# Optimization experiments

Hardware: AMD Instinct MI355X
Metric: run time of the kernel (lower is better)

## Reference

```python
import jax, jax.numpy as jnp
import numpy as np
import math

B, S, D, H, R, DFF = 4, 1024, 1024, 16, 64, 4096

def _layernorm(x, g, b, eps=1e-5):
    m = jnp.mean(x, axis=-1, keepdims=True)
    v = jnp.var(x, axis=-1, keepdims=True)
    return (x - m) / jnp.sqrt(v + eps) * g + b

def setup_inputs() -> dict:
    key = jax.random.key(0)
    ks = jax.random.split(key, 12)
    sc = 0.02
    return {
        "src": jax.random.normal(ks[0], (B, S, D), jnp.float32),
        "in_proj_w": jax.random.normal(ks[1], (3 * D, D), jnp.float32) * sc,
        "in_proj_b": jnp.zeros((3 * D,), jnp.float32),
        "out_proj_w": jax.random.normal(ks[2], (D, D), jnp.float32) * sc,
        "out_proj_b": jnp.zeros((D,), jnp.float32),
        "Qp_w": jax.random.normal(ks[3], (R, D), jnp.float32) * sc,
        "Qp_b": jnp.zeros((R,), jnp.float32),
        "Kp_w": jax.random.normal(ks[4], (R, D), jnp.float32) * sc,
        "Kp_b": jnp.zeros((R,), jnp.float32),
        "Vp_w": jax.random.normal(ks[5], (D, D), jnp.float32) * sc,
        "Vp_b": jnp.zeros((D,), jnp.float32),
        "lam": jnp.float32(0.5),
        "ff1_w": jax.random.normal(ks[6], (DFF, D), jnp.float32) * sc,
        "ff1_b": jnp.zeros((DFF,), jnp.float32),
        "ff2_w": jax.random.normal(ks[7], (D, DFF), jnp.float32) * sc,
        "ff2_b": jnp.zeros((D,), jnp.float32),
        "ln1_g": jnp.ones((D,), jnp.float32),
        "ln1_b": jnp.zeros((D,), jnp.float32),
        "ln2_g": jnp.ones((D,), jnp.float32),
        "ln2_b": jnp.zeros((D,), jnp.float32),
    }

def reference(src, in_proj_w, in_proj_b, out_proj_w, out_proj_b,
              Qp_w, Qp_b, Kp_w, Kp_b, Vp_w, Vp_b, lam,
              ff1_w, ff1_b, ff2_w, ff2_b, ln1_g, ln1_b, ln2_g, ln2_b):
    b, s, d = src.shape
    dh = d // H
    # ---- dense multi-head attention (torch nn.MultiheadAttention, eval) ----
    qkv = src @ in_proj_w.T + in_proj_b            # [B,S,3D]
    q, k, v = jnp.split(qkv, 3, axis=-1)
    q = q.reshape(b, s, H, dh).transpose(0, 2, 1, 3)  # [B,H,S,dh]
    k = k.reshape(b, s, H, dh).transpose(0, 2, 1, 3)
    v = v.reshape(b, s, H, dh).transpose(0, 2, 1, 3)
    scores = jnp.einsum('bhqd,bhkd->bhqk', q, k) / math.sqrt(dh)
    attn = jax.nn.softmax(scores, axis=-1)
    ctx = jnp.einsum('bhqk,bhkd->bhqd', attn, v)
    ctx = ctx.transpose(0, 2, 1, 3).reshape(b, s, d)
    dense_output = ctx @ out_proj_w.T + out_proj_b
    # ---- low-rank top-k sparse attention ----
    Q = src @ Qp_w.T + Qp_b                        # [B,S,R]
    K = src @ Kp_w.T + Kp_b
    V = src @ Vp_w.T + Vp_b                        # [B,S,D]
    QK = jnp.einsum('bqr,bkr->bqk', Q, K) / math.sqrt(R)
    aw = jax.nn.softmax(QK, axis=-1)               # [B,S,S]
    kk = max(1, int(s * 0.2))
    topv, topi = jax.lax.top_k(aw, kk)             # [B,S,kk]
    bi = jnp.arange(b)[:, None, None]
    si = jnp.arange(s)[None, :, None]
    sparse_attn = jnp.zeros_like(aw).at[bi, si, topi].set(topv)
    sparse_attn = sparse_attn / (jnp.sum(sparse_attn, axis=-1, keepdims=True) + 1e-9)
    sparse_output = jnp.einsum('bqk,bkd->bqd', sparse_attn, V)
    # ---- fuse, residual, norm, FFN ----
    sig = jax.nn.sigmoid(lam)
    fused = sig * dense_output + (1.0 - sig) * sparse_output
    x = _layernorm(src + fused, ln1_g, ln1_b)
    ff = jax.nn.relu(x @ ff1_w.T + ff1_b) @ ff2_w.T + ff2_b
    return _layernorm(x + ff, ln2_g, ln2_b)
```

## Files before the change

### kernel.cpp

```cpp
#include <hip/hip_runtime.h>
#include <hip/hip_bf16.h>
#include <math.h>
#include <type_traits>

typedef __hip_bfloat16 bf16;
typedef __attribute__((ext_vector_type(8))) short short8;
typedef __attribute__((ext_vector_type(4))) float f32x4;

#define NB 4
#define NS 1024
#define ND 1024
#define NH 16
#define NDH 64
#define NR 64
#define NDFF 4096
#define NM (NB*NS)
#define NTOPK 204

static __device__ __forceinline__ float b2f(bf16 x) { return __bfloat162float(x); }
static __device__ __forceinline__ bf16  f2b(float x) { return __float2bfloat16(x); }
static __device__ __forceinline__ unsigned short bfbits(float x) {
  bf16 h = __float2bfloat16(x);
  return *reinterpret_cast<unsigned short*>(&h);
}

static __device__ __forceinline__ void gload_lds16(const void* g, void* l) {
  __builtin_amdgcn_global_load_lds(
      (const __attribute__((address_space(1))) void*)g,
      (__attribute__((address_space(3))) void*)l, 16, 0, 0);
}

template<int N> static __device__ __forceinline__ void vm_wait() {
  if constexpr (N == 0)       asm volatile("s_waitcnt vmcnt(0)" ::: "memory");
  else if constexpr (N == 2)  asm volatile("s_waitcnt vmcnt(2)" ::: "memory");
  else if constexpr (N == 4)  asm volatile("s_waitcnt vmcnt(4)" ::: "memory");
  else if constexpr (N == 6)  asm volatile("s_waitcnt vmcnt(6)" ::: "memory");
  else if constexpr (N == 8)  asm volatile("s_waitcnt vmcnt(8)" ::: "memory");
  else static_assert(N == 0, "unsupported vmcnt");
}
static __device__ __forceinline__ void bar() {
  asm volatile("s_barrier" ::: "memory");
}

static __device__ __forceinline__ void ld8(const bf16* p, float* d) {
  const uint4 u = *(const uint4*)p;
  d[0] = __uint_as_float((u.x & 0xffffu) << 16);
  d[1] = __uint_as_float(u.x & 0xffff0000u);
  d[2] = __uint_as_float((u.y & 0xffffu) << 16);
  d[3] = __uint_as_float(u.y & 0xffff0000u);
  d[4] = __uint_as_float((u.z & 0xffffu) << 16);
  d[5] = __uint_as_float(u.z & 0xffff0000u);
  d[6] = __uint_as_float((u.w & 0xffffu) << 16);
  d[7] = __uint_as_float(u.w & 0xffff0000u);
}

static __device__ __forceinline__ float block_sum_256(float v, float* rbuf, int tid) {
  rbuf[tid] = v;
  __syncthreads();
  #pragma unroll
  for (int st = 128; st > 0; st >>= 1) {
    if (tid < st) rbuf[tid] += rbuf[tid + st];
    __syncthreads();
  }
  const float r = rbuf[0];
  __syncthreads();
  return r;
}

struct CastArgs {
  const float* in[6];
  bf16* out[6];
  unsigned end[6];
};
__global__ __launch_bounds__(256) void cast6_kernel(CastArgs a) {
  const unsigned b = blockIdx.x;
  int r = 0; unsigned base = 0;
  #pragma unroll
  for (int k = 0; k < 5; ++k)
    if (b >= a.end[k]) { r = k + 1; base = a.end[k]; }
  const float* in = a.in[r];
  bf16* out = a.out[r];
  const unsigned i = ((b - base) * 256 + threadIdx.x) * 4;
  const float4 v = *(const float4*)(in + i);
  uint2 o;
  o.x = (unsigned)bfbits(v.x) | ((unsigned)bfbits(v.y) << 16);
  o.y = (unsigned)bfbits(v.z) | ((unsigned)bfbits(v.w) << 16);
  *(uint2*)(out + i) = o;
}

__global__ __launch_bounds__(256) void pack_qk_kernel(
    const float* __restrict__ Qw, const float* __restrict__ Kw,
    const float* __restrict__ Qb, const float* __restrict__ Kb,
    bf16* __restrict__ w, float* __restrict__ bias) {
  const int r = blockIdx.x;
  const float* srcw = (r < 64) ? (Qw + (size_t)r * ND) : (Kw + (size_t)(r - 64) * ND);
  for (int i = threadIdx.x; i < ND; i += 256) w[(size_t)r * ND + i] = f2b(srcw[i]);
  if (r == 0)
    for (int i = threadIdx.x; i < 128; i += 256)
      bias[i] = (i < 64) ? Qb[i] : Kb[i - 64];
}

template<int BM, int BN, int BK, int BIAS, int RELU, int OUTF32, int OUTT, int VT>
__global__ __launch_bounds__(256) void mfma_gemm(
    const bf16* __restrict__ A, const bf16* __restrict__ W,
    const float* __restrict__ bias, void* __restrict__ C,
    int K, int lda, int ldb, int ldc,
    long long aHi, long long aLo, long long bHi, long long bLo,
    long long cHi, long long cLo, float scale, bf16* __restrict__ C2)
{
  constexpr int WTM = BM / 2;
  constexpr int WTN = BN / 2;
  constexpr int AM = WTM / 16;
  constexpr int AN = WTN / 16;
  constexpr int KK = BK / 32;
  constexpr int SLOTS = BK / 8;
  constexpr int RPC = 512 / BK;
  constexpr int LPW = (BM * BK) / 2048 + (BN * BK) / 2048;
  __shared__ short As[2][BM * BK];
  __shared__ short Bs[2][BN * BK];
  const int tid  = threadIdx.x;
  const int lane = tid & 63;
  const int w    = tid >> 6;
  const int z    = blockIdx.z;
  const long long aOff = (long long)(z >> 4) * aHi + (long long)(z & 15) * aLo;
  const long long bOff = (long long)(z >> 4) * bHi + (long long)(z & 15) * bLo;
  const long long cOff = (long long)(z >> 4) * cHi + (long long)(z & 15) * cLo;

  int bx = blockIdx.x, by = blockIdx.y;
  if ((gridDim.x & 7) == 0) {
    const unsigned lin = blockIdx.y * gridDim.x + blockIdx.x;
    const unsigned Wd = gridDim.x >> 3;
    const unsigned xcd = lin & 7, i = lin >> 3;
    bx = (int)(xcd * Wd + (i % Wd));
    by = (int)(i / Wd);
  }
  const int m0 = by * BM;
  const int n0 = bx * BN;
  const int wr = w >> 1, wc = w & 1;
  const int lm = lane & 15, quad = lane >> 4;

  f32x4 acc[AM][AN];
  #pragma unroll
  for (int i = 0; i < AM; ++i)
    #pragma unroll
    for (int j = 0; j < AN; ++j) acc[i][j] = (f32x4){0.f, 0.f, 0.f, 0.f};

  const int slot = lane & (SLOTS - 1);
  const int sr   = lane / SLOTS;
  const int swz  = (BK == 32) ? ((sr >> 1) & 3) : (sr & 7);
  const int scol = (slot ^ swz) << 3;
  const int xv   = (BK == 32) ? ((lm >> 1) & 3) : (lm & 7);
  const bf16* Ab = A + aOff;
  const bf16* Bb = W + bOff;

  auto stage = [&](int buf, int k0) {
    #pragma unroll
    for (int t = 0; t < (BM * BK) / 2048; ++t) {
      const int row = w * (BM / 4) + t * RPC;
      gload_lds16(Ab + (long long)(m0 + row + sr) * lda + k0 + scol, &As[buf][row * BK]);
    }
    #pragma unroll
    for (int t = 0; t < (BN * BK) / 2048; ++t) {
      const int row = w * (BN / 4) + t * RPC;
      gload_lds16(Bb + (long long)(n0 + row + sr) * ldb + k0 + scol, &Bs[buf][row * BK]);
    }
  };
  auto compute = [&](int buf) {
    #pragma unroll
    for (int kk = 0; kk < KK; ++kk) {
      const int cb = ((kk * 4 + quad) ^ xv) << 3;
      short8 af[AM], bfr[AN];
      #pragma unroll
      for (int i = 0; i < AM; ++i)
        af[i] = *(const short8*)&As[buf][(wr * WTM + i * 16 + lm) * BK + cb];
      #pragma unroll
      for (int j = 0; j < AN; ++j)
        bfr[j] = *(const short8*)&Bs[buf][(wc * WTN + j * 16 + lm) * BK + cb];
      #pragma unroll
      for (int i = 0; i < AM; ++i)
        #pragma unroll
        for (int j = 0; j < AN; ++j)
          acc[i][j] = __builtin_amdgcn_mfma_f32_16x16x32_bf16(af[i], bfr[j], acc[i][j], 0, 0, 0);
    }
  };

  stage(0, 0);
  int cur = 0;
  for (int k0 = BK; k0 < K; k0 += BK) {
    stage(cur ^ 1, k0);
    vm_wait<LPW>();
    bar();
    compute(cur);
    bar();
    cur ^= 1;
  }
  vm_wait<0>();
  bar();
  compute(cur);

  #pragma unroll
  for (int i = 0; i < AM; ++i) {
    #pragma unroll
    for (int j = 0; j < AN; ++j) {
      const int n = n0 + wc * WTN + j * 16 + lm;
      const float bj = BIAS ? bias[n] : 0.f;
      float v0 = acc[i][j][0] * scale + bj;
      float v1 = acc[i][j][1] * scale + bj;
      float v2 = acc[i][j][2] * scale + bj;
      float v3 = acc[i][j][3] * scale + bj;
      if (RELU) {
        v0 = fmaxf(v0, 0.f); v1 = fmaxf(v1, 0.f);
        v2 = fmaxf(v2, 0.f); v3 = fmaxf(v3, 0.f);
      }
      const int mm = m0 + wr * WTM + i * 16 + quad * 4;
      if (VT && n0 >= 2 * ND) {
        const int h = (n - 2 * ND) >> 6, d = (n - 2 * ND) & 63;
        uint2 u;
        u.x = (unsigned)bfbits(v0) | ((unsigned)bfbits(v1) << 16);
        u.y = (unsigned)bfbits(v2) | ((unsigned)bfbits(v3) << 16);
        bf16* dst = C2 + (long long)((mm >> 10) * NH + h) * (NDH * NS)
                       + (long long)d * NS + (mm & 1023);
        *(uint2*)dst = u;
      } else if (OUTT) {
        uint2 u;
        u.x = (unsigned)bfbits(v0) | ((unsigned)bfbits(v1) << 16);
        u.y = (unsigned)bfbits(v2) | ((unsigned)bfbits(v3) << 16);
        bf16* dst = (bf16*)C + cOff + (long long)(mm >> 10) * ((long long)ND * NS)
                       + (long long)n * NS + (mm & 1023);
        *(uint2*)dst = u;
      } else {
        const float vv[4] = {v0, v1, v2, v3};
        #pragma unroll
        for (int rr = 0; rr < 4; ++rr) {
          const long long co = cOff + (long long)(mm + rr) * ldc + n;
          if (OUTF32) ((float*)C)[co] = vv[rr];
          else        ((bf16*)C)[co] = f2b(vv[rr]);
        }
      }
    }
  }
}

template<int BIAS, int RELU, int VT>
__global__ __launch_bounds__(512) void mfma_gemm256(
    const bf16* __restrict__ A, const bf16* __restrict__ W,
    const float* __restrict__ bias, bf16* __restrict__ C,
    int K, int lda, int ldb, int ldc, bf16* __restrict__ C2)
{
  __shared__ short As[2][256 * 64];
  __shared__ short Bs[2][256 * 64];
  const int tid  = threadIdx.x;
  const int lane = tid & 63;
  const int w    = tid >> 6;
  int bx = blockIdx.x, by = blockIdx.y;
  if ((gridDim.x & 7) == 0) {
    const unsigned lin = blockIdx.y * gridDim.x + blockIdx.x;
    const unsigned Wd = gridDim.x >> 3;
    const unsigned xcd = lin & 7, i = lin >> 3;
    bx = (int)(xcd * Wd + (i % Wd));
    by = (int)(i / Wd);
  }
  const int m0 = by * 256;
  const int n0 = bx * 256;
  const int wr = w >> 2, wc = w & 3;
  const int lm = lane & 15, quad = lane >> 4;

  f32x4 acc[8][4];
  #pragma unroll
  for (int i = 0; i < 8; ++i)
    #pragma unroll
    for (int j = 0; j < 4; ++j) acc[i][j] = (f32x4){0.f, 0.f, 0.f, 0.f};

  const int slot = lane & 7, sr = lane >> 3;
  const int scol = (slot ^ sr) << 3;
  const int xv   = lm & 7;

  auto stgA = [&](int buf, int c, int k0) {
    gload_lds16(A + (long long)(m0 + c * 64 + w * 8 + sr) * lda + k0 + scol,
                &As[buf][(c * 64 + w * 8) * 64]);
  };
  auto stgB = [&](int buf, int c, int k0) {
    gload_lds16(W + (long long)(n0 + c * 64 + w * 8 + sr) * ldb + k0 + scol,
                &Bs[buf][(c * 64 + w * 8) * 64]);
  };
  auto dsA = [&](short8* afr, int h, int buf) {
    #pragma unroll
    for (int i = 0; i < 4; ++i)
      #pragma unroll
      for (int kk = 0; kk < 2; ++kk)
        afr[i * 2 + kk] = *(const short8*)
            &As[buf][(wr * 128 + h * 64 + i * 16 + lm) * 64 + (((kk * 4 + quad) ^ xv) << 3)];
  };
  auto dsB = [&](short8* bfr, int jh, int buf) {
    #pragma unroll
    for (int j = 0; j < 2; ++j)
      #pragma unroll
      for (int kk = 0; kk < 2; ++kk)
        bfr[j * 2 + kk] = *(const short8*)
            &Bs[buf][(wc * 64 + jh * 32 + j * 16 + lm) * 64 + (((kk * 4 + quad) ^ xv) << 3)];
  };
  auto mmaq = [&](auto H, auto JH, const short8* afr, const short8* bfr) {
    constexpr int h = decltype(H)::value, jh = decltype(JH)::value;
    __builtin_amdgcn_s_setprio(1);
    #pragma unroll
    for (int i = 0; i < 4; ++i)
      #pragma unroll
      for (int j = 0; j < 2; ++j)
        #pragma unroll
        for (int kk = 0; kk < 2; ++kk)
          acc[h * 4 + i][jh * 2 + j] = __builtin_amdgcn_mfma_f32_16x16x32_bf16(
              afr[i * 2 + kk], bfr[j * 2 + kk], acc[h * 4 + i][jh * 2 + j], 0, 0, 0);
    __builtin_amdgcn_s_setprio(0);
  };
  const std::integral_constant<int, 0> C0{};
  const std::integral_constant<int, 1> C1{};

  stgB(0, 0, 0); stgB(0, 1, 0); stgB(0, 2, 0); stgB(0, 3, 0);
  stgA(0, 0, 0); stgA(0, 2, 0); stgA(0, 1, 0); stgA(0, 3, 0);
  vm_wait<0>();
  bar();

  const int NT = K / 64;
  int p = 0;
  for (int kt = 0; kt < NT; ++kt, p ^= 1) {
    const int k1 = (kt + 1) * 64;
    const bool pre = (kt + 1 < NT);
    short8 afr[8], bfrA[4], bfrB[4];
    dsA(afr, 0, p); dsB(bfrA, 0, p);
    if (pre) { stgB(p ^ 1, 0, k1); stgB(p ^ 1, 1, k1); }
    bar();
    mmaq(C0, C0, afr, bfrA);
    bar();
    dsB(bfrB, 1, p);
    if (pre) { stgB(p ^ 1, 2, k1); stgB(p ^ 1, 3, k1); vm_wait<4>(); }
    else vm_wait<0>();
    bar();
    mmaq(C0, C1, afr, bfrB);
    bar();
    dsA(afr, 1, p);
    if (pre) { stgA(p ^ 1, 0, k1); stgA(p ^ 1, 2, k1); }
    bar();
    mmaq(C1, C0, afr, bfrA);
    bar();
    if (pre) { stgA(p ^ 1, 1, k1); stgA(p ^ 1, 3, k1); vm_wait<2>(); }
    else vm_wait<0>();
    bar();
    mmaq(C1, C1, afr, bfrB);
    bar();
  }

  #pragma unroll
  for (int i = 0; i < 8; ++i) {
    #pragma unroll
    for (int j = 0; j < 4; ++j) {
      const int n = n0 + wc * 64 + j * 16 + lm;
      const float bj = BIAS ? bias[n] : 0.f;
      float v0 = acc[i][j][0] + bj;
      float v1 = acc[i][j][1] + bj;
      float v2 = acc[i][j][2] + bj;
      float v3 = acc[i][j][3] + bj;
      if (RELU) {
        v0 = fmaxf(v0, 0.f); v1 = fmaxf(v1, 0.f);
        v2 = fmaxf(v2, 0.f); v3 = fmaxf(v3, 0.f);
      }
      const int mm = m0 + wr * 128 + i * 16 + quad * 4;
      if (VT && n0 >= 2 * ND) {
        const int h = (n - 2 * ND) >> 6, d = (n - 2 * ND) & 63;
        uint2 u;
        u.x = (unsigned)bfbits(v0) | ((unsigned)bfbits(v1) << 16);
        u.y = (unsigned)bfbits(v2) | ((unsigned)bfbits(v3) << 16);
        bf16* dst = C2 + (long long)((mm >> 10) * NH + h) * (NDH * NS)
                       + (long long)d * NS + (mm & 1023);
        *(uint2*)dst = u;
      } else {
        C[(long long)(mm + 0) * ldc + n] = f2b(v0);
        C[(long long)(mm + 1) * ldc + n] = f2b(v1);
        C[(long long)(mm + 2) * ldc + n] = f2b(v2);
        C[(long long)(mm + 3) * ldc + n] = f2b(v3);
      }
    }
  }
}

__global__ __launch_bounds__(256) void attn_kernel(
    const bf16* __restrict__ qkv,
    const bf16* __restrict__ Vt,
    bf16* __restrict__ ctx)
{
  __shared__ short smem[2][2][64 * 64];
  const int tid = threadIdx.x, lane = tid & 63, w = tid >> 6;
  const int lm = lane & 15, quad = lane >> 4;
  const int z = blockIdx.y, b = z >> 4, h = z & 15;
  const int q0 = blockIdx.x * 128;
  const bf16* Qb = qkv + (long long)b * NS * 3072 + h * 64;
  const bf16* Kb = Qb + ND;
  const bf16* Vb = Vt + (long long)z * (NDH * NS);

  short8 qf[2][2];
  #pragma unroll
  for (int j = 0; j < 2; ++j)
    #pragma unroll
    for (int kk = 0; kk < 2; ++kk)
      qf[j][kk] = *(const short8*)(Qb + (long long)(q0 + w * 32 + j * 16 + lm) * 3072
                                      + kk * 32 + quad * 8);

  const int slot = lane & 7, sr = lane >> 3;
  const int scol = (slot ^ sr) << 3;

  auto stage = [&](int buf, int t) {
    #pragma unroll
    for (int u = 0; u < 2; ++u) {
      const int row = w * 16 + u * 8;
      gload_lds16(Kb + (long long)(t * 64 + row + sr) * 3072 + scol,
                  &smem[buf][0][row * 64]);
    }
    #pragma unroll
    for (int u = 0; u < 2; ++u) {
      const int row = w * 16 + u * 8;
      gload_lds16(Vb + (long long)(row + sr) * NS + t * 64 + scol,
                  &smem[buf][1][row * 64]);
    }
  };

  f32x4 o[4][2];
  #pragma unroll
  for (int i = 0; i < 4; ++i)
    #pragma unroll
    for (int j = 0; j < 2; ++j) o[i][j] = (f32x4){0.f, 0.f, 0.f, 0.f};
  float m[2] = {-1e30f, -1e30f}, l[2] = {0.f, 0.f};

  stage(0, 0);
  for (int t = 0; t < 16; ++t) {
    const int buf = t & 1;
    if (t < 15) { stage(buf ^ 1, t + 1); vm_wait<4>(); }
    else        { vm_wait<0>(); }
    bar();

    f32x4 st[4][2];
    #pragma unroll
    for (int i = 0; i < 4; ++i)
      #pragma unroll
      for (int j = 0; j < 2; ++j) st[i][j] = (f32x4){0.f, 0.f, 0.f, 0.f};
    #pragma unroll
    for (int kk = 0; kk < 2; ++kk) {
      const int cb = ((kk * 4 + quad) ^ (lm & 7)) << 3;
      short8 ka[4];
      #pragma unroll
      for (int i = 0; i < 4; ++i)
        ka[i] = *(const short8*)&smem[buf][0][(i * 16 + lm) * 64 + cb];
      #pragma unroll
      for (int i = 0; i < 4; ++i)
        #pragma unroll
        for (int j = 0; j < 2; ++j)
          st[i][j] = __builtin_amdgcn_mfma_f32_16x16x32_bf16(ka[i], qf[j][kk], st[i][j], 0, 0, 0);
    }

    #pragma unroll
    for (int j = 0; j < 2; ++j) {
      float pm = -1e30f;
      #pragma unroll
      for (int i = 0; i < 4; ++i)
        #pragma unroll
        for (int r = 0; r < 4; ++r) {
          st[i][j][r] *= 0.125f;
          pm = fmaxf(pm, st[i][j][r]);
        }
      pm = fmaxf(pm, __shfl_xor(pm, 16, 64));
      pm = fmaxf(pm, __shfl_xor(pm, 32, 64));
      const float mn = fmaxf(m[j], pm);
      const float sc = __expf(m[j] - mn);
      float ps = 0.f;
      #pragma unroll
      for (int i = 0; i < 4; ++i)
        #pragma unroll
        for (int r = 0; r < 4; ++r) {
          const float e = __expf(st[i][j][r] - mn);
          st[i][j][r] = e;
          ps += e;
        }
      ps += __shfl_xor(ps, 16, 64);
      ps += __shfl_xor(ps, 32, 64);
      l[j] = l[j] * sc + ps;
      m[j] = mn;
      #pragma unroll
      for (int i = 0; i < 4; ++i)
        #pragma unroll
        for (int r = 0; r < 4; ++r) o[i][j][r] *= sc;
    }

    unsigned u0[4][2], u1[4][2];
    #pragma unroll
    for (int i = 0; i < 4; ++i)
      #pragma unroll
      for (int j = 0; j < 2; ++j) {
        u0[i][j] = (unsigned)bfbits(st[i][j][0]) | ((unsigned)bfbits(st[i][j][1]) << 16);
        u1[i][j] = (unsigned)bfbits(st[i][j][2]) | ((unsigned)bfbits(st[i][j][3]) << 16);
      }
    const int s0l = ((quad & 1) * 2) * 16 + lm;
    const int s1l = s0l + 16;
    const bool hi = (quad >> 1) != 0;

    #pragma unroll
    for (int kk = 0; kk < 2; ++kk) {
      short8 pf[2];
      #pragma unroll
      for (int j = 0; j < 2; ++j) {
        const unsigned a0 = __shfl(u0[kk * 2][j],     s0l, 64);
        const unsigned a1 = __shfl(u1[kk * 2][j],     s0l, 64);
        const unsigned b0 = __shfl(u0[kk * 2 + 1][j], s0l, 64);
        const unsigned b1 = __shfl(u1[kk * 2 + 1][j], s0l, 64);
        const unsigned c0 = __shfl(u0[kk * 2][j],     s1l, 64);
        const unsigned c1 = __shfl(u1[kk * 2][j],     s1l, 64);
        const unsigned d0 = __shfl(u0[kk * 2 + 1][j], s1l, 64);
        const unsigned d1 = __shfl(u1[kk * 2 + 1][j], s1l, 64);
        union { uint4 u; short8 s; } cv;
        cv.u.x = hi ? b0 : a0; cv.u.y = hi ? b1 : a1;
        cv.u.z = hi ? d0 : c0; cv.u.w = hi ? d1 : c1;
        pf[j] = cv.s;
      }
      const int cb = ((kk * 4 + quad) ^ (lm & 7)) << 3;
      short8 va[4];
      #pragma unroll
      for (int i = 0; i < 4; ++i)
        va[i] = *(const short8*)&smem[buf][1][(i * 16 + lm) * 64 + cb];
      #pragma unroll
      for (int i = 0; i < 4; ++i)
        #pragma unroll
        for (int j = 0; j < 2; ++j)
          o[i][j] = __builtin_amdgcn_mfma_f32_16x16x32_bf16(va[i], pf[j], o[i][j], 0, 0, 0);
    }
    bar();
  }

  short (*OL)[72] = (short(*)[72])&smem[0][0][0];
  #pragma unroll
  for (int j = 0; j < 2; ++j) {
    const float inv = 1.f / l[j];
    #pragma unroll
    for (int i = 0; i < 4; ++i) {
      uint2 u;
      u.x = (unsigned)bfbits(o[i][j][0] * inv) | ((unsigned)bfbits(o[i][j][1] * inv) << 16);
      u.y = (unsigned)bfbits(o[i][j][2] * inv) | ((unsigned)bfbits(o[i][j][3] * inv) << 16);
      *(uint2*)&OL[w * 32 + j * 16 + lm][i * 16 + quad * 4] = u;
    }
  }
  __syncthreads();
  {
    const int q = tid >> 1, c = (tid & 1) * 32;
    const uint4 r0 = *(const uint4*)&OL[q][c];
    const uint4 r1 = *(const uint4*)&OL[q][c + 8];
    const uint4 r2 = *(const uint4*)&OL[q][c + 16];
    const uint4 r3 = *(const uint4*)&OL[q][c + 24];
    bf16* dst = ctx + ((long long)(b * NS + q0 + q)) * 1024 + h * 64 + c;
    ((uint4*)dst)[0] = r0; ((uint4*)dst)[1] = r1;
    ((uint4*)dst)[2] = r2; ((uint4*)dst)[3] = r3;
  }
}

__global__ __launch_bounds__(256) void sparse_select_kernel(
    const float* __restrict__ S, bf16* __restrict__ aw)
{
  __shared__ unsigned hist[4][256];
  const int tid = threadIdx.x;
  const int lane = tid & 63;
  const int wv = tid >> 6;
  const long long row = (long long)blockIdx.x * 4 + wv;

  float sv[16];
  const float* sp = S + row * 1024 + lane * 16;
  #pragma unroll
  for (int c = 0; c < 4; ++c) {
    const float4 v = ((const float4*)sp)[c];
    sv[4*c] = v.x; sv[4*c+1] = v.y; sv[4*c+2] = v.z; sv[4*c+3] = v.w;
  }
  unsigned key[16];
  #pragma unroll
  for (int j = 0; j < 16; ++j) {
    const unsigned u = __float_as_uint(sv[j]);
    key[j] = (u & 0x80000000u) ? ~u : (u | 0x80000000u);
  }

  unsigned pref = 0u;
  int need = NTOPK;
  #pragma unroll
  for (int p = 3; p >= 0; --p) {
    *(uint4*)&hist[wv][lane * 4] = (uint4){0u, 0u, 0u, 0u};
    __syncthreads();
    const int sh = (p + 1) * 8;
    #pragma unroll
    for (int j = 0; j < 16; ++j) {
      const bool part = (p == 3) || ((key[j] >> sh) == pref);
      if (part) atomicAdd(&hist[wv][(key[j] >> (p * 8)) & 255u], 1u);
    }
    __syncthreads();
    const unsigned h0 = hist[wv][4*lane],     h1 = hist[wv][4*lane + 1];
    const unsigned h2 = hist[wv][4*lane + 2], h3 = hist[wv][4*lane + 3];
    const unsigned s3 = h3, s2 = h2 + s3, s1 = h1 + s2, s0 = h0 + s1;
    unsigned sum = s0;
    #pragma unroll
    for (int d2 = 1; d2 < 64; d2 <<= 1) {
      const unsigned t = __shfl_down(sum, d2, 64);
      if (lane < 64 - d2) sum += t;
    }
    const unsigned above = sum - s0;
    const unsigned cum[4]  = {above + s0, above + s1, above + s2, above + s3};
    const unsigned next[4] = {above + s1, above + s2, above + s3, above};
    unsigned candPref = 0u; int candNeed = 0; bool has = false;
    #pragma unroll
    for (int i = 0; i < 4; ++i) {
      if ((int)cum[i] >= need && (int)next[i] < need) {
        has = true;
        candPref = (pref << 8) | (unsigned)(4 * lane + i);
        candNeed = need - (int)next[i];
      }
    }
    const unsigned long long m = __ballot(has);
    const int srcLane = (int)(__ffsll((long long)m) - 1);
    pref = (unsigned)__shfl((int)candPref, srcLane, 64);
    need = __shfl(candNeed, srcLane, 64);
  }

  const unsigned T = pref;
  const unsigned tb = (T & 0x80000000u) ? (T ^ 0x80000000u) : ~T;
  const float thr = __uint_as_float(tb);

  float wvv[16];
  float psTop = 0.f, psAll = 0.f;
  #pragma unroll
  for (int j = 0; j < 16; ++j) {
    const float e = __expf(sv[j] - thr);
    psAll += e;
    const float wt = (key[j] >= T) ? e : 0.f;
    psTop += wt;
    wvv[j] = wt;
  }
  #pragma unroll
  for (int s = 1; s < 64; s <<= 1) {
    psTop += __shfl_xor(psTop, s, 64);
    psAll += __shfl_xor(psAll, s, 64);
  }
  const float inv = 1.f / (psTop + 1e-9f * psAll);

  uint4 o0, o1;
  o0.x = (unsigned)bfbits(wvv[0]*inv)  | ((unsigned)bfbits(wvv[1]*inv)  << 16);
  o0.y = (unsigned)bfbits(wvv[2]*inv)  | ((unsigned)bfbits(wvv[3]*inv)  << 16);
  o0.z = (unsigned)bfbits(wvv[4]*inv)  | ((unsigned)bfbits(wvv[5]*inv)  << 16);
  o0.w = (unsigned)bfbits(wvv[6]*inv)  | ((unsigned)bfbits(wvv[7]*inv)  << 16);
  o1.x = (unsigned)bfbits(wvv[8]*inv)  | ((unsigned)bfbits(wvv[9]*inv)  << 16);
  o1.y = (unsigned)bfbits(wvv[10]*inv) | ((unsigned)bfbits(wvv[11]*inv) << 16);
  o1.z = (unsigned)bfbits(wvv[12]*inv) | ((unsigned)bfbits(wvv[13]*inv) << 16);
  o1.w = (unsigned)bfbits(wvv[14]*inv) | ((unsigned)bfbits(wvv[15]*inv) << 16);
  bf16* op = aw + row * 1024 + lane * 16;
  ((uint4*)op)[0] = o0; ((uint4*)op)[1] = o1;
}

__global__ __launch_bounds__(256) void fuse_ln1_kernel(
    const float* __restrict__ src, const bf16* __restrict__ dense,
    const bf16* __restrict__ sparse, const float* __restrict__ lam,
    const float* __restrict__ g, const float* __restrict__ beta,
    bf16* __restrict__ x1)
{
  __shared__ float y[ND];
  __shared__ float rbuf[256];
  const int tid = threadIdx.x;
  const size_t base = (size_t)blockIdx.x * ND;
  const float sig = 1.f / (1.f + __expf(-lam[0]));
  const float c1 = 1.f - sig;
  float s1 = 0.f, s2 = 0.f;
  #pragma unroll
  for (int j = 0; j < 4; ++j) {
    const int i = tid + (j << 8);
    const float v = src[base + i] + sig * b2f(dense[base + i]) + c1 * b2f(sparse[base + i]);
    y[i] = v; s1 += v; s2 += v * v;
  }
  const float sum1 = block_sum_256(s1, rbuf, tid);
  const float sum2 = block_sum_256(s2, rbuf, tid);
  const float mean = sum1 * (1.f / ND);
  const float var  = sum2 * (1.f / ND) - mean * mean;
  const float rstd = rsqrtf(var + 1e-5f);
  #pragma unroll
  for (int j = 0; j < 4; ++j) {
    const int i = tid + (j << 8);
    x1[base + i] = f2b((y[i] - mean) * rstd * g[i] + beta[i]);
  }
}

__global__ __launch_bounds__(256) void ln2_kernel(
    const bf16* __restrict__ x1, const bf16* __restrict__ ff,
    const float* __restrict__ g, const float* __restrict__ beta,
    float* __restrict__ outp)
{
  __shared__ float y[ND];
  __shared__ float rbuf[256];
  const int tid = threadIdx.x;
  const size_t base = (size_t)blockIdx.x * ND;
  float s1 = 0.f, s2 = 0.f;
  #pragma unroll
  for (int j = 0; j < 4; ++j) {
    const int i = tid + (j << 8);
    const float v = b2f(x1[base + i]) + b2f(ff[base + i]);
    y[i] = v; s1 += v; s2 += v * v;
  }
  const float sum1 = block_sum_256(s1, rbuf, tid);
  const float sum2 = block_sum_256(s2, rbuf, tid);
  const float mean = sum1 * (1.f / ND);
  const float var  = sum2 * (1.f / ND) - mean * mean;
  const float rstd = rsqrtf(var + 1e-5f);
  #pragma unroll
  for (int j = 0; j < 4; ++j) {
    const int i = tid + (j << 8);
    outp[base + i] = (y[i] - mean) * rstd * g[i] + beta[i];
  }
}

extern "C" void kernel_launch(void* const* d_in, const int* in_sizes, int n_in,
                              void* d_out, int out_size, void* d_ws, size_t ws_size,
                              hipStream_t stream)
{
  const float* src        = (const float*)d_in[0];
  const float* in_proj_w  = (const float*)d_in[1];
  const float* in_proj_b  = (const float*)d_in[2];
  const float* out_proj_w = (const float*)d_in[3];
  const float* out_proj_b = (const float*)d_in[4];
  const float* Qp_w  = (const float*)d_in[5];
  const float* Qp_b  = (const float*)d_in[6];
  const float* Kp_w  = (const float*)d_in[7];
  const float* Kp_b  = (const float*)d_in[8];
  const float* Vp_w  = (const float*)d_in[9];
  const float* Vp_b  = (const float*)d_in[10];
  const float* lam   = (const float*)d_in[11];
  const float* ff1_w = (const float*)d_in[12];
  const float* ff1_b = (const float*)d_in[13];
  const float* ff2_w = (const float*)d_in[14];
  const float* ff2_b = (const float*)d_in[15];
  const float* ln1_g = (const float*)d_in[16];
  const float* ln1_b = (const float*)d_in[17];
  const float* ln2_g = (const float*)d_in[18];
  const float* ln2_b = (const float*)d_in[19];
  (void)in_sizes; (void)n_in; (void)out_size; (void)ws_size;

  char* ws = (char*)d_ws;
  size_t off = 0;
  auto take = [&](size_t bytes) -> void* {
    void* p = ws + off; off += (bytes + 255) & ~(size_t)255; return p;
  };
  bf16*  src_bf  = (bf16*) take((size_t)NM * ND * 2);
  bf16*  w_qkv   = (bf16*) take((size_t)3 * ND * ND * 2);
  bf16*  w_out   = (bf16*) take((size_t)ND * ND * 2);
  bf16*  w_vp    = (bf16*) take((size_t)ND * ND * 2);
  bf16*  w_ff1   = (bf16*) take((size_t)NDFF * ND * 2);
  bf16*  w_ff2   = (bf16*) take((size_t)ND * NDFF * 2);
  bf16*  w_qk    = (bf16*) take((size_t)128 * ND * 2);
  float* bias_qk = (float*)take(128 * 4);
  const size_t mark = off;
  bf16*  qkv     = (bf16*) take((size_t)NM * 3 * ND * 2);
  bf16*  Vt_all  = (bf16*) take((size_t)NH * NS * NS * 2);
  bf16*  Vt_old  = (bf16*) take((size_t)NH * NDH * NS * 2);
  bf16*  ctx     = (bf16*) take((size_t)NM * ND * 2);
  bf16*  dense   = (bf16*) take((size_t)NM * ND * 2);
  bf16*  QKs_bf  = (bf16*) take((size_t)NM * 128 * 2);
  bf16*  Vsp     = (bf16*) take((size_t)NM * ND * 2);
  bf16*  sparse  = (bf16*) take((size_t)NM * ND * 2);
  (void)Vt_old; (void)Vsp;
  bf16*  x1    = (bf16*)(ws + mark);
  bf16*  h1    = (bf16*)(ws + mark + (size_t)NM * ND * 2);
  bf16*  ffout = (bf16*)(ws + mark + (size_t)NM * ND * 2 + (size_t)NM * NDFF * 2);
  bf16*  aw    = (bf16*)(ws + mark + 2 * (size_t)NM * ND * 2 + (size_t)NM * NDFF * 2);
  float* S_sp  = (float*)(ws + mark + (size_t)NM * ND * 2);
  bf16*  Vsp_t = (bf16*)ctx;

  const dim3 blk(256);
  bf16* const NOC2 = nullptr;
  {
    CastArgs a;
    a.in[0] = src;        a.out[0] = src_bf;
    a.in[1] = in_proj_w;  a.out[1] = w_qkv;
    a.in[2] = out_proj_w; a.out[2] = w_out;
    a.in[3] = Vp_w;       a.out[3] = w_vp;
    a.in[4] = ff1_w;      a.out[4] = w_ff1;
    a.in[5] = ff2_w;      a.out[5] = w_ff2;
    a.end[0] = 4096; a.end[1] = 7168; a.end[2] = 8192;
    a.end[3] = 9216; a.end[4] = 13312; a.end[5] = 17408;
    cast6_kernel<<<dim3(17408), blk, 0, stream>>>(a);
  }
  pack_qk_kernel<<<dim3(128), blk, 0, stream>>>(Qp_w, Kp_w, Qp_b, Kp_b, w_qk, bias_qk);

  mfma_gemm256<1,0,1><<<dim3(3*ND/256, NM/256), dim3(512), 0, stream>>>(
      src_bf, w_qkv, in_proj_b, qkv, ND, ND, ND, 3*ND, Vt_all);

  attn_kernel<<<dim3(NS/128, NB*NH), blk, 0, stream>>>(qkv, Vt_all, ctx);

  mfma_gemm<128,64,64,1,0,0,0,0><<<dim3(ND/64, NM/128, 1), blk, 0, stream>>>(
      ctx, w_out, out_proj_b, dense, ND, ND, ND, ND, 0,0, 0,0, 0,0, 1.f, NOC2);
  mfma_gemm<128,64,64,1,0,0,0,0><<<dim3(2, NM/128, 1), blk, 0, stream>>>(
      src_bf, w_qk, bias_qk, QKs_bf, ND, ND, ND, 128, 0,0, 0,0, 0,0, 1.f, NOC2);
  mfma_gemm<128,64,64,0,0,1,0,0><<<dim3(NS/64, NS/128, NB), blk, 0, stream>>>(
      QKs_bf, QKs_bf + 64, nullptr, S_sp, 64, 128, 128, NS,
      0, (long long)NS*128, 0, (long long)NS*128, 0, (long long)NS*NS, 0.125f, NOC2);
  mfma_gemm<128,64,64,1,0,0,1,0><<<dim3(ND/64, NM/128, 1), blk, 0, stream>>>(
      src_bf, w_vp, Vp_b, Vsp_t, ND, ND, ND, NS, 0,0, 0,0, 0,0, 1.f, NOC2);
  sparse_select_kernel<<<dim3(NM/4), blk, 0, stream>>>(S_sp, aw);
  mfma_gemm<128,64,64,0,0,0,0,0><<<dim3(ND/64, NS/128, NB), blk, 0, stream>>>(
      aw, Vsp_t, nullptr, sparse, NS, NS, NS, ND,
      0, (long long)NS*ND, 0, (long long)ND*NS, 0, (long long)NS*ND, 1.f, NOC2);
  fuse_ln1_kernel<<<dim3(NM), blk, 0, stream>>>(src, dense, sparse, lam, ln1_g, ln1_b, x1);
  mfma_gemm256<1,1,0><<<dim3(NDFF/256, NM/256), dim3(512), 0, stream>>>(
      x1, w_ff1, ff1_b, h1, ND, ND, ND, NDFF, NOC2);
  mfma_gemm<128,64,64,1,0,0,0,0><<<dim3(ND/64, NM/128, 1), blk, 0, stream>>>(
      h1, w_ff2, ff2_b, ffout, NDFF, NDFF, NDFF, ND, 0,0, 0,0, 0,0, 1.f, NOC2);
  ln2_kernel<<<dim3(NM), blk, 0, stream>>>(x1, ffout, ln2_g, ln2_b, (float*)d_out);
}
```

Measured before the change: 424.3 us.

## Pre-pack B operands into MFMA fragment layout and load them directly to registers

Adds a pack kernel that casts the out_proj, Vp and ff2 weights into a layout that matches 16x32 MFMA fragments. A new GEMM variant reads these packed B tiles straight from global memory into registers with one 16-byte load per lane, and stages only A through LDS. The Vp projection now writes its output in the same packed layout, so the sparse-attention GEMM can use the same path. This removes LDS staging and bank traffic for B and shrinks the general cast kernel, at the cost of extra pack launches and B loads that are less coalesced.

```diff
diff --git a/kernel.cpp b/kernel.cpp
--- a/kernel.cpp
+++ b/kernel.cpp
@@ -88,6 +88,23 @@
   *(uint2*)(out + i) = o;
 }
 
+__global__ __launch_bounds__(256) void pack_w_kernel(
+    const float* __restrict__ W, bf16* __restrict__ out, int K) {
+  const int lane = threadIdx.x & 63, sub = threadIdx.x >> 6;
+  const int kt2 = blockIdx.x * 4 + sub;
+  const int nt  = blockIdx.y;
+  const int lm = lane & 15, quad = lane >> 4;
+  const float* p = W + (size_t)(nt * 16 + lm) * K + kt2 * 32 + quad * 8;
+  const float4 a = *(const float4*)p;
+  const float4 b = *(const float4*)(p + 4);
+  uint4 o;
+  o.x = (unsigned)bfbits(a.x) | ((unsigned)bfbits(a.y) << 16);
+  o.y = (unsigned)bfbits(a.z) | ((unsigned)bfbits(a.w) << 16);
+  o.z = (unsigned)bfbits(b.x) | ((unsigned)bfbits(b.y) << 16);
+  o.w = (unsigned)bfbits(b.z) | ((unsigned)bfbits(b.w) << 16);
+  *(uint4*)(out + (((size_t)(nt * (K >> 5) + kt2)) << 9) + lane * 8) = o;
+}
+
 __global__ __launch_bounds__(256) void pack_qk_kernel(
     const float* __restrict__ Qw, const float* __restrict__ Kw,
     const float* __restrict__ Qb, const float* __restrict__ Kb,
@@ -100,13 +117,13 @@
       bias[i] = (i < 64) ? Qb[i] : Kb[i - 64];
 }
 
-template<int BM, int BN, int BK, int BIAS, int RELU, int OUTF32, int OUTT, int VT>
+template<int BM, int BN, int BK, int BIAS, int RELU, int OUTF32>
 __global__ __launch_bounds__(256) void mfma_gemm(
     const bf16* __restrict__ A, const bf16* __restrict__ W,
     const float* __restrict__ bias, void* __restrict__ C,
     int K, int lda, int ldb, int ldc,
     long long aHi, long long aLo, long long bHi, long long bLo,
-    long long cHi, long long cLo, float scale, bf16* __restrict__ C2)
+    long long cHi, long long cLo, float scale)
 {
   constexpr int WTM = BM / 2;
   constexpr int WTN = BN / 2;
@@ -204,38 +221,136 @@
     for (int j = 0; j < AN; ++j) {
       const int n = n0 + wc * WTN + j * 16 + lm;
       const float bj = BIAS ? bias[n] : 0.f;
-      float v0 = acc[i][j][0] * scale + bj;
-      float v1 = acc[i][j][1] * scale + bj;
-      float v2 = acc[i][j][2] * scale + bj;
-      float v3 = acc[i][j][3] * scale + bj;
+      #pragma unroll
+      for (int rr = 0; rr < 4; ++rr) {
+        const int m = m0 + wr * WTM + i * 16 + quad * 4 + rr;
+        float v = acc[i][j][rr] * scale + bj;
+        if (RELU) v = fmaxf(v, 0.f);
+        const long long co = cOff + (long long)m * ldc + n;
+        if (OUTF32) ((float*)C)[co] = v;
+        else        ((bf16*)C)[co] = f2b(v);
+      }
+    }
+  }
+}
+
+template<int BIAS, int RELU, int PACKOUT>
+__global__ __launch_bounds__(256) void mfma_gemm_pb(
+    const bf16* __restrict__ A, const bf16* __restrict__ Bp,
+    const float* __restrict__ bias, bf16* __restrict__ C,
+    int K, int lda, int ldc,
+    long long aLo, long long bLo, long long cLo)
+{
+  __shared__ short As[2][128 * 64];
+  const int tid = threadIdx.x, lane = tid & 63, w = tid >> 6;
+  const int z = blockIdx.z;
+  const long long aOff = (long long)z * aLo;
+  const long long cOff = (long long)z * cLo;
+  int bx = blockIdx.x, by = blockIdx.y;
+  if ((gridDim.x & 7) == 0) {
+    const unsigned lin = blockIdx.y * gridDim.x + blockIdx.x;
+    const unsigned Wd = gridDim.x >> 3;
+    const unsigned xcd = lin & 7, i = lin >> 3;
+    bx = (int)(xcd * Wd + (i % Wd));
+    by = (int)(i / Wd);
+  }
+  const int m0 = by * 128, n0 = bx * 64;
+  const int wr = w >> 1, wc = w & 1;
+  const int lm = lane & 15, quad = lane >> 4;
+  const int KT2 = K >> 5;
+
+  f32x4 acc[4][2];
+  #pragma unroll
+  for (int i = 0; i < 4; ++i)
+    #pragma unroll
+    for (int j = 0; j < 2; ++j) acc[i][j] = (f32x4){0.f, 0.f, 0.f, 0.f};
+
+  const int slot = lane & 7, sr = lane >> 3;
+  const int scol = (slot ^ sr) << 3;
+  const int xv   = lm & 7;
+  const bf16* Ab = A + aOff;
+  const bf16* Bb = Bp + (long long)z * bLo
+                 + (((long long)(n0 / 16 + wc * 2) * KT2) << 9) + lane * 8;
+
+  auto stageA = [&](int buf, int t) {
+    const int k0 = t * 64;
+    #pragma unroll
+    for (int u = 0; u < 4; ++u) {
+      const int row = w * 32 + u * 8;
+      gload_lds16(Ab + (long long)(m0 + row + sr) * lda + k0 + scol, &As[buf][row * 64]);
+    }
+  };
+  short8 brg[2][4];
+  auto loadB = [&](auto BUF, int t) {
+    constexpr int bu = decltype(BUF)::value;
+    #pragma unroll
+    for (int j = 0; j < 2; ++j)
+      #pragma unroll
+      for (int kk = 0; kk < 2; ++kk)
+        brg[bu][j * 2 + kk] =
+            *(const short8*)(Bb + (((long long)j * KT2 + t * 2 + kk) << 9));
+  };
+  auto compute = [&](auto BUF) {
+    constexpr int bu = decltype(BUF)::value;
+    #pragma unroll
+    for (int kk = 0; kk < 2; ++kk) {
+      const int cb = ((kk * 4 + quad) ^ xv) << 3;
+      short8 af[4];
+      #pragma unroll
+      for (int i = 0; i < 4; ++i)
+        af[i] = *(const short8*)&As[bu][(wr * 64 + i * 16 + lm) * 64 + cb];
+      #pragma unroll
+      for (int i = 0; i < 4; ++i)
+        #pragma unroll
+        for (int j = 0; j < 2; ++j)
+          acc[i][j] = __builtin_amdgcn_mfma_f32_16x16x32_bf16(
+              af[i], brg[bu][j * 2 + kk], acc[i][j], 0, 0, 0);
+    }
+  };
+  const std::integral_constant<int, 0> B0{};
+  const std::integral_constant<int, 1> B1{};
+
+  const int nt = K / 64;
+  stageA(0, 0); loadB(B0, 0);
+  for (int t = 1; t + 1 < nt; t += 2) {
+    stageA(1, t);     loadB(B1, t);
+    vm_wait<8>(); bar(); compute(B0); bar();
+    stageA(0, t + 1); loadB(B0, t + 1);
+    vm_wait<8>(); bar(); compute(B1); bar();
+  }
+  stageA(1, nt - 1); loadB(B1, nt - 1);
+  vm_wait<8>(); bar(); compute(B0); bar();
+  vm_wait<0>(); bar(); compute(B1);
+
+  #pragma unroll
+  for (int i = 0; i < 4; ++i) {
+    #pragma unroll
+    for (int j = 0; j < 2; ++j) {
+      const int n = n0 + wc * 32 + j * 16 + lm;
+      const float bj = BIAS ? bias[n] : 0.f;
+      float v0 = acc[i][j][0] + bj;
+      float v1 = acc[i][j][1] + bj;
+      float v2 = acc[i][j][2] + bj;
+      float v3 = acc[i][j][3] + bj;
       if (RELU) {
         v0 = fmaxf(v0, 0.f); v1 = fmaxf(v1, 0.f);
         v2 = fmaxf(v2, 0.f); v3 = fmaxf(v3, 0.f);
       }
-      const int mm = m0 + wr * WTM + i * 16 + quad * 4;
-      if (VT && n0 >= 2 * ND) {
-        const int h = (n - 2 * ND) >> 6, d = (n - 2 * ND) & 63;
+      const int mm = m0 + wr * 64 + i * 16 + quad * 4;
+      if (PACKOUT) {
+        const int b = mm >> 10, s = mm & 1023;
+        bf16* dst = C + (long long)b * ((long long)NS * ND)
+                  + (((long long)(n >> 4) * (NS >> 5) + (s >> 5)) << 9)
+                  + (((s >> 3) & 3) * 16 + (n & 15)) * 8 + (s & 7);
         uint2 u;
         u.x = (unsigned)bfbits(v0) | ((unsigned)bfbits(v1) << 16);
         u.y = (unsigned)bfbits(v2) | ((unsigned)bfbits(v3) << 16);
-        bf16* dst = C2 + (long long)((mm >> 10) * NH + h) * (NDH * NS)
-                       + (long long)d * NS + (mm & 1023);
-        *(uint2*)dst = u;
-      } else if (OUTT) {
-        uint2 u;
-        u.x = (unsigned)bfbits(v0) | ((unsigned)bfbits(v1) << 16);
-        u.y = (unsigned)bfbits(v2) | ((unsigned)bfbits(v3) << 16);
-        bf16* dst = (bf16*)C + cOff + (long long)(mm >> 10) * ((long long)ND * NS)
-                       + (long long)n * NS + (mm & 1023);
         *(uint2*)dst = u;
       } else {
-        const float vv[4] = {v0, v1, v2, v3};
-        #pragma unroll
-        for (int rr = 0; rr < 4; ++rr) {
-          const long long co = cOff + (long long)(mm + rr) * ldc + n;
-          if (OUTF32) ((float*)C)[co] = vv[rr];
-          else        ((bf16*)C)[co] = f2b(vv[rr]);
-        }
+        C[cOff + (long long)(mm + 0) * ldc + n] = f2b(v0);
+        C[cOff + (long long)(mm + 1) * ldc + n] = f2b(v1);
+        C[cOff + (long long)(mm + 2) * ldc + n] = f2b(v2);
+        C[cOff + (long long)(mm + 3) * ldc + n] = f2b(v3);
       }
     }
   }
@@ -746,10 +861,10 @@
   };
   bf16*  src_bf  = (bf16*) take((size_t)NM * ND * 2);
   bf16*  w_qkv   = (bf16*) take((size_t)3 * ND * ND * 2);
-  bf16*  w_out   = (bf16*) take((size_t)ND * ND * 2);
-  bf16*  w_vp    = (bf16*) take((size_t)ND * ND * 2);
+  bf16*  w_out_p = (bf16*) take((size_t)ND * ND * 2);
+  bf16*  w_vp_p  = (bf16*) take((size_t)ND * ND * 2);
   bf16*  w_ff1   = (bf16*) take((size_t)NDFF * ND * 2);
-  bf16*  w_ff2   = (bf16*) take((size_t)ND * NDFF * 2);
+  bf16*  w_ff2_p = (bf16*) take((size_t)ND * NDFF * 2);
   bf16*  w_qk    = (bf16*) take((size_t)128 * ND * 2);
   float* bias_qk = (float*)take(128 * 4);
   const size_t mark = off;
@@ -767,7 +882,7 @@
   bf16*  ffout = (bf16*)(ws + mark + (size_t)NM * ND * 2 + (size_t)NM * NDFF * 2);
   bf16*  aw    = (bf16*)(ws + mark + 2 * (size_t)NM * ND * 2 + (size_t)NM * NDFF * 2);
   float* S_sp  = (float*)(ws + mark + (size_t)NM * ND * 2);
-  bf16*  Vsp_t = (bf16*)ctx;
+  bf16*  Vsp_pk = (bf16*)ctx;
 
   const dim3 blk(256);
   bf16* const NOC2 = nullptr;
@@ -775,14 +890,17 @@
     CastArgs a;
     a.in[0] = src;        a.out[0] = src_bf;
     a.in[1] = in_proj_w;  a.out[1] = w_qkv;
-    a.in[2] = out_proj_w; a.out[2] = w_out;
-    a.in[3] = Vp_w;       a.out[3] = w_vp;
-    a.in[4] = ff1_w;      a.out[4] = w_ff1;
-    a.in[5] = ff2_w;      a.out[5] = w_ff2;
-    a.end[0] = 4096; a.end[1] = 7168; a.end[2] = 8192;
-    a.end[3] = 9216; a.end[4] = 13312; a.end[5] = 17408;
-    cast6_kernel<<<dim3(17408), blk, 0, stream>>>(a);
-  }
+    a.in[2] = ff1_w;      a.out[2] = w_ff1;
+    a.in[3] = src;        a.out[3] = src_bf;
+    a.in[4] = src;        a.out[4] = src_bf;
+    a.in[5] = src;        a.out[5] = src_bf;
+    a.end[0] = 4096; a.end[1] = 7168; a.end[2] = 11264;
+    a.end[3] = 11264; a.end[4] = 11264; a.end[5] = 11264;
+    cast6_kernel<<<dim3(11264), blk, 0, stream>>>(a);
+  }
+  pack_w_kernel<<<dim3(ND/128,   ND/16), blk, 0, stream>>>(out_proj_w, w_out_p, ND);
+  pack_w_kernel<<<dim3(ND/128,   ND/16), blk, 0, stream>>>(Vp_w,       w_vp_p,  ND);
+  pack_w_kernel<<<dim3(NDFF/128, ND/16), blk, 0, stream>>>(ff2_w,      w_ff2_p, NDFF);
   pack_qk_kernel<<<dim3(128), blk, 0, stream>>>(Qp_w, Kp_w, Qp_b, Kp_b, w_qk, bias_qk);
 
   mfma_gemm256<1,0,1><<<dim3(3*ND/256, NM/256), dim3(512), 0, stream>>>(
@@ -790,23 +908,23 @@
 
   attn_kernel<<<dim3(NS/128, NB*NH), blk, 0, stream>>>(qkv, Vt_all, ctx);
 
-  mfma_gemm<128,64,64,1,0,0,0,0><<<dim3(ND/64, NM/128, 1), blk, 0, stream>>>(
-      ctx, w_out, out_proj_b, dense, ND, ND, ND, ND, 0,0, 0,0, 0,0, 1.f, NOC2);
-  mfma_gemm<128,64,64,1,0,0,0,0><<<dim3(2, NM/128, 1), blk, 0, stream>>>(
-      src_bf, w_qk, bias_qk, QKs_bf, ND, ND, ND, 128, 0,0, 0,0, 0,0, 1.f, NOC2);
-  mfma_gemm<128,64,64,0,0,1,0,0><<<dim3(NS/64, NS/128, NB), blk, 0, stream>>>(
+  mfma_gemm_pb<1,0,0><<<dim3(ND/64, NM/128, 1), blk, 0, stream>>>(
+      ctx, w_out_p, out_proj_b, dense, ND, ND, ND, 0, 0, 0);
+  mfma_gemm<128,64,64,1,0,0><<<dim3(2, NM/128, 1), blk, 0, stream>>>(
+      src_bf, w_qk, bias_qk, QKs_bf, ND, ND, ND, 128, 0,0, 0,0, 0,0, 1.f);
+  mfma_gemm<128,64,64,0,0,1><<<dim3(NS/64, NS/128, NB), blk, 0, stream>>>(
       QKs_bf, QKs_bf + 64, nullptr, S_sp, 64, 128, 128, NS,
-      0, (long long)NS*128, 0, (long long)NS*128, 0, (long long)NS*NS, 0.125f, NOC2);
-  mfma_gemm<128,64,64,1,0,0,1,0><<<dim3(ND/64, NM/128, 1), blk, 0, stream>>>(
-      src_bf, w_vp, Vp_b, Vsp_t, ND, ND, ND, NS, 0,0, 0,0, 0,0, 1.f, NOC2);
+      0, (long long)NS*128, 0, (long long)NS*128, 0, (long long)NS*NS, 0.125f);
+  mfma_gemm_pb<1,0,1><<<dim3(ND/64, NM/128, 1), blk, 0, stream>>>(
+      src_bf, w_vp_p, Vp_b, Vsp_pk, ND, ND, 0, 0, 0, 0);
   sparse_select_kernel<<<dim3(NM/4), blk, 0, stream>>>(S_sp, aw);
-  mfma_gemm<128,64,64,0,0,0,0,0><<<dim3(ND/64, NS/128, NB), blk, 0, stream>>>(
-      aw, Vsp_t, nullptr, sparse, NS, NS, NS, ND,
-      0, (long long)NS*ND, 0, (long long)ND*NS, 0, (long long)NS*ND, 1.f, NOC2);
+  mfma_gemm_pb<0,0,0><<<dim3(ND/64, NS/128, NB), blk, 0, stream>>>(
+      aw, Vsp_pk, nullptr, sparse, NS, NS, ND,
+      (long long)NS*ND, (long long)NS*ND, (long long)NS*ND);
   fuse_ln1_kernel<<<dim3(NM), blk, 0, stream>>>(src, dense, sparse, lam, ln1_g, ln1_b, x1);
   mfma_gemm256<1,1,0><<<dim3(NDFF/256, NM/256), dim3(512), 0, stream>>>(
       x1, w_ff1, ff1_b, h1, ND, ND, ND, NDFF, NOC2);
-  mfma_gemm<128,64,64,1,0,0,0,0><<<dim3(ND/64, NM/128, 1), blk, 0, stream>>>(
-      h1, w_ff2, ff2_b, ffout, NDFF, NDFF, NDFF, ND, 0,0, 0,0, 0,0, 1.f, NOC2);
+  mfma_gemm_pb<1,0,0><<<dim3(ND/64, NM/128, 1), blk, 0, stream>>>(
+      h1, w_ff2_p, ff2_b, ffout, NDFF, NDFF, ND, 0, 0, 0);
   ln2_kernel<<<dim3(NM), blk, 0, stream>>>(x1, ffout, ln2_g, ln2_b, (float*)d_out);
 }
```

After: 421.4 us. No clear change (-0.7%).
